# Kernel tuning notes

Hardware: AMD Instinct MI355X
Metric: run time of the kernel (lower is better)

The kernel has to match this reference:

```python
import jax, jax.numpy as jnp
import numpy as np

NUM_LEVEL = 16
LOG_T = 19
TABLE_SIZE = 2 ** LOG_T
FEAT = 2
MIN_RES = 16
MAX_RES = 512
N_POINTS = 262144

# [Teschner et al. 2003] spatial hash primes, wrapped to int32 like torch does
HASH_COEFFS = jnp.asarray(np.array([1, 2654435761, 805459861], dtype=np.uint32).astype(np.int32))


def _resolutions():
    coeff = (MAX_RES / MIN_RES) ** (1.0 / (NUM_LEVEL - 1))
    return jnp.floor(MIN_RES * (jnp.float32(coeff) ** jnp.arange(NUM_LEVEL, dtype=jnp.float32)))


def _spatial_hash(verts_i32):
    # verts_i32: (..., 3) int32; wrap-around int32 multiply then xor, then mod T (non-negative)
    x = HASH_COEFFS * verts_i32
    idx = jnp.bitwise_xor(jnp.bitwise_xor(x[..., 0], x[..., 1]), x[..., 2])
    return jnp.mod(idx, TABLE_SIZE)


def _hash_encode(coords, tables):
    # coords: (N,3) f32 in [0,1); tables: (L,T,F) f16
    res = _resolutions()                                   # (L,)
    scaled = coords[None, :, :] * res[:, None, None]        # (L,N,3)
    floor = jnp.floor(scaled)
    ceil = jnp.ceil(scaled)
    # 8 voxel corners via floor/ceil selection bits
    offs = jnp.asarray(np.array([[(o >> 2) & 1, (o >> 1) & 1, o & 1] for o in range(8)], dtype=np.bool_))
    sel = offs[:, None, None, :]                            # (8,1,1,3)
    corner = jnp.where(sel, ceil[None], floor[None])        # (8,L,N,3)
    comp = jnp.where(sel, floor[None], ceil[None])          # opposite corner (8,L,N,3)
    idx = _spatial_hash(corner.astype(jnp.int32))           # (8,L,N)
    # gather per-level features: tables[l][idx[:,l,:]] -> (L,8,N,F)
    feats = jax.vmap(lambda tab, i: tab[i], in_axes=(0, 1))(tables, idx)
    # trilinear weight of corner o = prod |opposite_corner - scaled|
    w = jnp.prod(jnp.abs(comp - scaled[None]), axis=-1)     # (8,L,N)
    w = jnp.transpose(w, (1, 0, 2))                         # (L,8,N)
    lvl = jnp.sum(feats.astype(jnp.float32) * w[..., None], axis=1)  # (L,N,F)
    return jnp.transpose(lvl, (1, 0, 2)).reshape(coords.shape[0], NUM_LEVEL * FEAT)


def _mlp(x, w_in, b_in, w_h0, b_h0, w_h1, b_h1, w_out, b_out):
    h = jax.nn.relu(x @ w_in.T + b_in)
    h = jax.nn.relu(h @ w_h0.T + b_h0)
    h = jax.nn.relu(h @ w_h1.T + b_h1)
    return h @ w_out.T + b_out


def setup_inputs() -> dict:
    key = jax.random.key(0)
    ks = jax.random.split(key, 8)
    coords = jax.random.uniform(ks[0], (N_POINTS, 3), dtype=jnp.float32)
    tables = (2e-4 * jax.random.uniform(ks[1], (NUM_LEVEL, TABLE_SIZE, FEAT), dtype=jnp.float32) - 1e-4).astype(jnp.float16)
    def lin(k, out_d, in_d):
        return jax.random.normal(k, (out_d, in_d), dtype=jnp.float32) * (1.0 / np.sqrt(in_d))
    return {
        'coords': coords, 'tables': tables,
        'w_in': lin(ks[2], 64, 32), 'b_in': jnp.zeros((64,), jnp.float32),
        'w_h0': lin(ks[3], 64, 64), 'b_h0': jnp.zeros((64,), jnp.float32),
        'w_h1': lin(ks[4], 64, 64), 'b_h1': jnp.zeros((64,), jnp.float32),
        'w_out': lin(ks[5], 16, 64), 'b_out': jnp.zeros((16,), jnp.float32),
    }


def reference(coords, tables, w_in, b_in, w_h0, b_h0, w_h1, b_h1, w_out, b_out):
    enc = _hash_encode(coords, tables)  # (N, 32)
    return _mlp(enc, w_in, b_in, w_h0, b_h0, w_h1, b_h1, w_out, b_out)  # (N, 16)
```

## Files before the change

kernel.cpp:

```cpp
#include <hip/hip_runtime.h>

#define NLVL 16
#define LOGT 19
#define TMASK ((1u << LOGT) - 1u)
#define SCALE 4096.0f
#define INV_SCALE (1.0f / 4096.0f)
#define NFRAG 22

typedef _Float16 half_t;
typedef half_t half8 __attribute__((ext_vector_type(8)));
typedef half_t half4 __attribute__((ext_vector_type(4)));
typedef half_t half2v __attribute__((ext_vector_type(2)));
typedef float  float4v __attribute__((ext_vector_type(4)));

__device__ __constant__ float RES_C[NLVL] = {16.f, 20.f, 25.f, 32.f, 40.f, 50.f, 64.f, 80.f,
                                             101.f, 128.f, 161.f, 203.f, 256.f, 322.f, 406.f, 512.f};

__device__ __forceinline__ float4v mfma16(half8 a, half8 b, float4v c) {
    return __builtin_amdgcn_mfma_f32_16x16x32_f16(a, b, c, 0, 0, 0);
}

__global__ __launch_bounds__(64, 1) void nerf_wprep(
    const float* __restrict__ w_in, const float* __restrict__ w_h0,
    const float* __restrict__ w_h1, const float* __restrict__ w_out,
    half8* __restrict__ frags)
{
    const int frag = blockIdx.x;
    const int lane = threadIdx.x;
    const int m    = lane & 15;
    const int quad = lane >> 4;

    const float* W; int ncol, row, col;
    if (frag < 4)       { W = w_in;  ncol = 32; row = frag * 16 + m;            col = quad * 8; }
    else if (frag < 12) { const int f = frag - 4;
                          W = w_h0;  ncol = 64; row = (f >> 1) * 16 + m;        col = (f & 1) * 32 + quad * 8; }
    else if (frag < 20) { const int f = frag - 12;
                          W = w_h1;  ncol = 64; row = (f >> 1) * 16 + m;        col = (f & 1) * 32 + quad * 8; }
    else                { const int f = frag - 20;
                          W = w_out; ncol = 64; row = m;                        col = f * 32 + quad * 8; }

    const float* p = W + row * ncol + col;
    half8 r;
    #pragma unroll
    for (int j = 0; j < 8; ++j) r[j] = (half_t)p[j];
    frags[frag * 64 + lane] = r;
}

__global__ __launch_bounds__(256, 8) void nerf_encode_pin(
    const float* __restrict__ coords,
    const float2* __restrict__ tab,
    half_t* __restrict__ encT, int npts)
{
    const int b    = blockIdx.x;
    const int half = (int)(gridDim.x >> 1);
    const int hi   = (b >= half) ? 1 : 0;
    const int l    = (b & 7) + (hi << 3);
    const int pb   = (hi ? (b - half) : b) >> 3;

    const int side = threadIdx.x & 1;
    const int base = pb * 256 + (threadIdx.x >> 1);
    const int p0 = base, p1 = base + 128;

    const float r = RES_C[l];
    const float2* __restrict__ bp = tab + (((unsigned)l) << LOGT);

    const float ax = coords[p0 * 3 + 0] * r, ay = coords[p0 * 3 + 1] * r, az = coords[p0 * 3 + 2] * r;
    const float afx = floorf(ax), afy = floorf(ay), afz = floorf(az);
    const float agx = ceilf(ax),  agy = ceilf(ay),  agz = ceilf(az);
    const unsigned ahx = side ? (unsigned)(int)agx : (unsigned)(int)afx;
    const float    awx = side ? (ax - afx) : (agx - ax);
    const unsigned ahfy = (unsigned)(int)afy * 2654435761u;
    const unsigned ahgy = (unsigned)(int)agy * 2654435761u;
    const unsigned ahfz = (unsigned)(int)afz * 805459861u;
    const unsigned ahgz = (unsigned)(int)agz * 805459861u;
    const float aty = ay - afy, atz = az - afz, auy = agy - ay, auz = agz - az;

    const float bx = coords[p1 * 3 + 0] * r, by = coords[p1 * 3 + 1] * r, bz = coords[p1 * 3 + 2] * r;
    const float bfx = floorf(bx), bfy = floorf(by), bfz = floorf(bz);
    const float bgx = ceilf(bx),  bgy = ceilf(by),  bgz = ceilf(bz);
    const unsigned bhx = side ? (unsigned)(int)bgx : (unsigned)(int)bfx;
    const float    bwx = side ? (bx - bfx) : (bgx - bx);
    const unsigned bhfy = (unsigned)(int)bfy * 2654435761u;
    const unsigned bhgy = (unsigned)(int)bgy * 2654435761u;
    const unsigned bhfz = (unsigned)(int)bfz * 805459861u;
    const unsigned bhgz = (unsigned)(int)bgz * 805459861u;
    const float bty = by - bfy, btz = bz - bfz, buy = bgy - by, buz = bgz - bz;

    const float2 a0 = bp[(ahx ^ ahfy ^ ahfz) & TMASK];
    const float2 a1 = bp[(ahx ^ ahfy ^ ahgz) & TMASK];
    const float2 a2 = bp[(ahx ^ ahgy ^ ahfz) & TMASK];
    const float2 a3 = bp[(ahx ^ ahgy ^ ahgz) & TMASK];
    const float2 b0 = bp[(bhx ^ bhfy ^ bhfz) & TMASK];
    const float2 b1 = bp[(bhx ^ bhfy ^ bhgz) & TMASK];
    const float2 b2 = bp[(bhx ^ bhgy ^ bhfz) & TMASK];
    const float2 b3 = bp[(bhx ^ bhgy ^ bhgz) & TMASK];

    const float aw0 = awx * auy * auz, aw1 = awx * auy * atz;
    const float aw2 = awx * aty * auz, aw3 = awx * aty * atz;
    const float bw0 = bwx * buy * buz, bw1 = bwx * buy * btz;
    const float bw2 = bwx * bty * buz, bw3 = bwx * bty * btz;

    float ae0 = aw0 * a0.x + aw1 * a1.x + aw2 * a2.x + aw3 * a3.x;
    float ae1 = aw0 * a0.y + aw1 * a1.y + aw2 * a2.y + aw3 * a3.y;
    float be0 = bw0 * b0.x + bw1 * b1.x + bw2 * b2.x + bw3 * b3.x;
    float be1 = bw0 * b0.y + bw1 * b1.y + bw2 * b2.y + bw3 * b3.y;

    ae0 += __shfl_xor(ae0, 1, 64);
    ae1 += __shfl_xor(ae1, 1, 64);
    be0 += __shfl_xor(be0, 1, 64);
    be1 += __shfl_xor(be1, 1, 64);

    if (side == 0) {
        half2v h0; h0[0] = (half_t)(ae0 * SCALE); h0[1] = (half_t)(ae1 * SCALE);
        half2v h1; h1[0] = (half_t)(be0 * SCALE); h1[1] = (half_t)(be1 * SCALE);
        *reinterpret_cast<half2v*>(&encT[((size_t)l * npts + p0) * 2]) = h0;
        *reinterpret_cast<half2v*>(&encT[((size_t)l * npts + p1) * 2]) = h1;
    }
}

__global__ __launch_bounds__(256, 2) void nerf_mlp4(
    const half_t* __restrict__ encT,
    const half8* __restrict__ frags,
    const float* __restrict__ b_in, const float* __restrict__ b_h0,
    const float* __restrict__ b_h1, const float* __restrict__ b_out,
    float* __restrict__ out, int npts)
{
    __shared__ half_t actS[4][64 * 64];

    const int t    = threadIdx.x;
    const int lane = t & 63;
    const int wv   = t >> 6;
    const int m    = lane & 15;
    const int quad = lane >> 4;

    const size_t pbase = (size_t)blockIdx.x * 256 + (size_t)wv * 64;

    half8 be[4];
    #pragma unroll
    for (int T = 0; T < 4; ++T) {
        #pragma unroll
        for (int d = 0; d < 4; ++d) {
            const int L = quad * 4 + d;
            const half2v v = *reinterpret_cast<const half2v*>(
                &encT[((size_t)L * npts + pbase + T * 16 + m) * 2]);
            be[T][d * 2 + 0] = v[0];
            be[T][d * 2 + 1] = v[1];
        }
    }

    half8 aL1[4], aL2[8], aL3[8], aL4[2];
    #pragma unroll
    for (int f = 0; f < 4; ++f) aL1[f] = frags[(0 + f) * 64 + lane];
    #pragma unroll
    for (int f = 0; f < 8; ++f) aL2[f] = frags[(4 + f) * 64 + lane];
    #pragma unroll
    for (int f = 0; f < 8; ++f) aL3[f] = frags[(12 + f) * 64 + lane];
    #pragma unroll
    for (int f = 0; f < 2; ++f) aL4[f] = frags[(20 + f) * 64 + lane];

    float4v bL1[4], bL2[4], bL3[4], bL4;
    #pragma unroll
    for (int mt = 0; mt < 4; ++mt) {
        bL1[mt] = *reinterpret_cast<const float4v*>(b_in + mt * 16 + quad * 4);
        bL2[mt] = *reinterpret_cast<const float4v*>(b_h0 + mt * 16 + quad * 4);
        bL3[mt] = *reinterpret_cast<const float4v*>(b_h1 + mt * 16 + quad * 4);
    }
    bL4 = *reinterpret_cast<const float4v*>(b_out + quad * 4);

    half_t* const buf = &actS[wv][0];
    const float4v zero = {0.f, 0.f, 0.f, 0.f};

    auto storeTile = [&](int lp, int mt, float4v acc, float4v bias) {
        half4 h4;
        #pragma unroll
        for (int r = 0; r < 4; ++r)
            h4[r] = (half_t)fmaxf(fmaf(bias[r], SCALE, acc[r]), 0.f);
        const int c16  = mt * 2 + (quad >> 1);
        const int phys = c16 ^ (lp & 7);
        *reinterpret_cast<half4*>(&buf[lp * 64 + phys * 8 + (quad & 1) * 4]) = h4;
    };
    auto loadB = [&](int lp, int h) -> half8 {
        const int phys = (h * 4 + quad) ^ (lp & 7);
        return *reinterpret_cast<const half8*>(&buf[lp * 64 + phys * 8]);
    };

    #pragma unroll
    for (int T = 0; T < 4; ++T) {
        const int lp = T * 16 + m;
        #pragma unroll
        for (int mt = 0; mt < 4; ++mt) {
            float4v acc = mfma16(aL1[mt], be[T], zero);
            storeTile(lp, mt, acc, bL1[mt]);
        }
    }
    #pragma unroll
    for (int T = 0; T < 4; ++T) {
        const int lp = T * 16 + m;
        const half8 p0 = loadB(lp, 0);
        const half8 p1 = loadB(lp, 1);
        #pragma unroll
        for (int mt = 0; mt < 4; ++mt) {
            float4v acc = mfma16(aL2[mt * 2 + 0], p0, zero);
            acc         = mfma16(aL2[mt * 2 + 1], p1, acc);
            storeTile(lp, mt, acc, bL2[mt]);
        }
    }
    #pragma unroll
    for (int T = 0; T < 4; ++T) {
        const int lp = T * 16 + m;
        const half8 p0 = loadB(lp, 0);
        const half8 p1 = loadB(lp, 1);
        #pragma unroll
        for (int mt = 0; mt < 4; ++mt) {
            float4v acc = mfma16(aL3[mt * 2 + 0], p0, zero);
            acc         = mfma16(aL3[mt * 2 + 1], p1, acc);
            storeTile(lp, mt, acc, bL3[mt]);
        }
    }
    #pragma unroll
    for (int T = 0; T < 4; ++T) {
        const int lp = T * 16 + m;
        const half8 p0 = loadB(lp, 0);
        const half8 p1 = loadB(lp, 1);
        float4v acc = mfma16(aL4[0], p0, zero);
        acc         = mfma16(aL4[1], p1, acc);
        float4v res;
        #pragma unroll
        for (int r = 0; r < 4; ++r)
            res[r] = fmaf(acc[r], INV_SCALE, bL4[r]);
        *reinterpret_cast<float4v*>(out + (pbase + lp) * 16 + quad * 4) = res;
    }
}

__global__ __launch_bounds__(256, 2) void nerf_fused(
    const float* __restrict__ coords,
    const float2* __restrict__ tab,
    const float* __restrict__ w_in, const float* __restrict__ b_in,
    const float* __restrict__ w_h0, const float* __restrict__ b_h0,
    const float* __restrict__ w_h1, const float* __restrict__ b_h1,
    const float* __restrict__ w_out, const float* __restrict__ b_out,
    float* __restrict__ out, int npts)
{
    __shared__ half_t encS[256 * 40];
    __shared__ half_t actS[4][2][32 * 64];

    const int t    = threadIdx.x;
    const int lane = t & 63;
    const int wv   = t >> 6;
    const int m    = lane & 15;
    const int quad = lane >> 4;
    const int pt = blockIdx.x * 256 + t;

    {
        const float cx = coords[pt * 3 + 0];
        const float cy = coords[pt * 3 + 1];
        const float cz = coords[pt * 3 + 2];
        float enc[32];
        #pragma unroll
        for (int l = 0; l < NLVL; ++l) {
            const float r = RES_C[l];
            const float sx = cx * r, sy = cy * r, sz = cz * r;
            const float fx = floorf(sx), fy = floorf(sy), fz = floorf(sz);
            const float gx = ceilf(sx),  gy = ceilf(sy),  gz = ceilf(sz);
            const unsigned hfx = (unsigned)(int)fx;
            const unsigned hgx = (unsigned)(int)gx;
            const unsigned hfy = (unsigned)(int)fy * 2654435761u;
            const unsigned hgy = (unsigned)(int)gy * 2654435761u;
            const unsigned hfz = (unsigned)(int)fz * 805459861u;
            const unsigned hgz = (unsigned)(int)gz * 805459861u;
            const float tx = sx - fx, ty = sy - fy, tz = sz - fz;
            const float ux = gx - sx, uy = gy - sy, uz = gz - sz;
            const unsigned lbase = ((unsigned)l) << LOGT;
            float e0 = 0.f, e1 = 0.f;
            #pragma unroll
            for (int o = 0; o < 8; ++o) {
                const unsigned h = ((o & 4) ? hgx : hfx)
                                 ^ ((o & 2) ? hgy : hfy)
                                 ^ ((o & 1) ? hgz : hfz);
                const unsigned idx = h & TMASK;
                const float w = (((o & 4) ? tx : ux)
                              *  ((o & 2) ? ty : uy))
                              *  ((o & 1) ? tz : uz);
                const float2 fv = tab[lbase + idx];
                e0 = fmaf(w, fv.x, e0);
                e1 = fmaf(w, fv.y, e1);
            }
            enc[2 * l + 0] = e0;
            enc[2 * l + 1] = e1;
        }
        #pragma unroll
        for (int c = 0; c < 4; ++c) {
            half8 h8;
            #pragma unroll
            for (int j = 0; j < 8; ++j) h8[j] = (half_t)(enc[c * 8 + j] * SCALE);
            *reinterpret_cast<half8*>(&encS[t * 40 + c * 8]) = h8;
        }
    }

    auto loadA = [&](const float* __restrict__ W, int ncol, int row, int col) -> half8 {
        const float* p = W + row * ncol + col;
        const float4v lo = *reinterpret_cast<const float4v*>(p);
        const float4v hi = *reinterpret_cast<const float4v*>(p + 4);
        half8 r;
        r[0] = (half_t)lo[0]; r[1] = (half_t)lo[1]; r[2] = (half_t)lo[2]; r[3] = (half_t)lo[3];
        r[4] = (half_t)hi[0]; r[5] = (half_t)hi[1]; r[6] = (half_t)hi[2]; r[7] = (half_t)hi[3];
        return r;
    };

    half8 aL1[4], aL2[8], aL3[8], aL4[2];
    #pragma unroll
    for (int mt = 0; mt < 4; ++mt) aL1[mt] = loadA(w_in, 32, mt * 16 + m, quad * 8);
    #pragma unroll
    for (int mt = 0; mt < 4; ++mt) {
        aL2[mt * 2 + 0] = loadA(w_h0, 64, mt * 16 + m, 0 * 32 + quad * 8);
        aL2[mt * 2 + 1] = loadA(w_h0, 64, mt * 16 + m, 1 * 32 + quad * 8);
        aL3[mt * 2 + 0] = loadA(w_h1, 64, mt * 16 + m, 0 * 32 + quad * 8);
        aL3[mt * 2 + 1] = loadA(w_h1, 64, mt * 16 + m, 1 * 32 + quad * 8);
    }
    aL4[0] = loadA(w_out, 64, m, 0 * 32 + quad * 8);
    aL4[1] = loadA(w_out, 64, m, 1 * 32 + quad * 8);

    float4v bL1[4], bL2[4], bL3[4], bL4;
    #pragma unroll
    for (int mt = 0; mt < 4; ++mt) {
        bL1[mt] = *reinterpret_cast<const float4v*>(b_in + mt * 16 + quad * 4);
        bL2[mt] = *reinterpret_cast<const float4v*>(b_h0 + mt * 16 + quad * 4);
        bL3[mt] = *reinterpret_cast<const float4v*>(b_h1 + mt * 16 + quad * 4);
    }
    bL4 = *reinterpret_cast<const float4v*>(b_out + quad * 4);

    half_t* const ping = &actS[wv][0][0];
    half_t* const pong = &actS[wv][1][0];
    const float4v zero = {0.f, 0.f, 0.f, 0.f};

    auto storeTile = [&](half_t* buf, int lp, int mt, float4v acc, float4v bias) {
        half4 h4;
        #pragma unroll
        for (int r = 0; r < 4; ++r)
            h4[r] = (half_t)fmaxf(fmaf(bias[r], SCALE, acc[r]), 0.f);
        const int c16  = mt * 2 + (quad >> 1);
        const int phys = c16 ^ (lp & 7);
        *reinterpret_cast<half4*>(&buf[lp * 64 + phys * 8 + (quad & 1) * 4]) = h4;
    };
    auto loadB = [&](half_t* buf, int lp, int h) -> half8 {
        const int phys = (h * 4 + quad) ^ (lp & 7);
        return *reinterpret_cast<const half8*>(&buf[lp * 64 + phys * 8]);
    };

    for (int g = 0; g < 2; ++g) {
        #pragma unroll
        for (int nt = 0; nt < 2; ++nt) {
            const int lp   = nt * 16 + m;
            const int prow = wv * 64 + g * 32 + lp;
            const half8 bfr = *reinterpret_cast<const half8*>(&encS[prow * 40 + quad * 8]);
            #pragma unroll
            for (int mt = 0; mt < 4; ++mt) {
                float4v acc = mfma16(aL1[mt], bfr, zero);
                storeTile(ping, lp, mt, acc, bL1[mt]);
            }
            {
                const half8 p0 = loadB(ping, lp, 0);
                const half8 p1 = loadB(ping, lp, 1);
                #pragma unroll
                for (int mt = 0; mt < 4; ++mt) {
                    float4v acc = mfma16(aL2[mt * 2 + 0], p0, zero);
                    acc         = mfma16(aL2[mt * 2 + 1], p1, acc);
                    storeTile(pong, lp, mt, acc, bL2[mt]);
                }
            }
            {
                const half8 p0 = loadB(pong, lp, 0);
                const half8 p1 = loadB(pong, lp, 1);
                #pragma unroll
                for (int mt = 0; mt < 4; ++mt) {
                    float4v acc = mfma16(aL3[mt * 2 + 0], p0, zero);
                    acc         = mfma16(aL3[mt * 2 + 1], p1, acc);
                    storeTile(ping, lp, mt, acc, bL3[mt]);
                }
            }
            {
                const half8 p0 = loadB(ping, lp, 0);
                const half8 p1 = loadB(ping, lp, 1);
                float4v acc = mfma16(aL4[0], p0, zero);
                acc         = mfma16(aL4[1], p1, acc);
                float4v res;
                #pragma unroll
                for (int r = 0; r < 4; ++r)
                    res[r] = fmaf(acc[r], INV_SCALE, bL4[r]);
                const size_t ptg = (size_t)blockIdx.x * 256 + (size_t)wv * 64 + g * 32 + lp;
                *reinterpret_cast<float4v*>(out + ptg * 16 + quad * 4) = res;
            }
        }
    }
}

extern "C" void kernel_launch(void* const* d_in, const int* in_sizes, int n_in,
                              void* d_out, int out_size, void* d_ws, size_t ws_size,
                              hipStream_t stream) {
    const float*  coords = (const float*)d_in[0];
    const float2* tables = (const float2*)d_in[1];
    const float*  w_in   = (const float*)d_in[2];
    const float*  b_in   = (const float*)d_in[3];
    const float*  w_h0   = (const float*)d_in[4];
    const float*  b_h0   = (const float*)d_in[5];
    const float*  w_h1   = (const float*)d_in[6];
    const float*  b_h1   = (const float*)d_in[7];
    const float*  w_out  = (const float*)d_in[8];
    const float*  b_out  = (const float*)d_in[9];
    float* out = (float*)d_out;

    const int npts = in_sizes[0] / 3;
    const size_t encBytes  = (size_t)npts * 32 * sizeof(half_t);
    const size_t fragBytes = (size_t)NFRAG * 64 * sizeof(half8);

    if (ws_size >= encBytes + fragBytes && (npts & 255) == 0) {
        half_t* encT  = (half_t*)d_ws;
        half8*  frags = (half8*)((char*)d_ws + encBytes);
        nerf_wprep<<<NFRAG, 64, 0, stream>>>(w_in, w_h0, w_h1, w_out, frags);
        const int bpl = npts >> 8;
        nerf_encode_pin<<<bpl * NLVL, 256, 0, stream>>>(coords, tables, encT, npts);
        nerf_mlp4<<<npts / 256, 256, 0, stream>>>(encT, frags,
                                                  b_in, b_h0, b_h1, b_out,
                                                  out, npts);
    } else {
        nerf_fused<<<npts / 256, 256, 0, stream>>>(coords, tables,
                                                   w_in, b_in, w_h0, b_h0,
                                                   w_h1, b_h1, w_out, b_out,
                                                   out, npts);
    }
}
```

Measured before the change: 195.8 us.

## Keep MLP activations in registers via cross-lane shuffle transpose instead of LDS

The MLP kernel drops its per-wave shared-memory activation buffer. Each layer's MFMA accumulator is converted to ReLU'd fp16 pairs and rearranged into the next layer's B-operand layout with two xor-shuffles per register. Bias is folded into the MFMA accumulator init, and launch bounds are raised to allow more waves per CU. This removes LDS store/load round trips between layers, in exchange for extra shuffle and select instructions and possible register pressure at the higher occupancy target.

```diff
diff --git a/kernel.cpp b/kernel.cpp
--- a/kernel.cpp
+++ b/kernel.cpp
@@ -12,6 +12,7 @@
 typedef half_t half4 __attribute__((ext_vector_type(4)));
 typedef half_t half2v __attribute__((ext_vector_type(2)));
 typedef float  float4v __attribute__((ext_vector_type(4)));
+typedef unsigned int uint4v __attribute__((ext_vector_type(4)));
 
 __device__ __constant__ float RES_C[NLVL] = {16.f, 20.f, 25.f, 32.f, 40.f, 50.f, 64.f, 80.f,
                                              101.f, 128.f, 161.f, 203.f, 256.f, 322.f, 406.f, 512.f};
@@ -118,21 +119,56 @@
     }
 }
 
-__global__ __launch_bounds__(256, 2) void nerf_mlp4(
+__device__ __forceinline__ unsigned pack_relu2(float x, float y) {
+    half2v h;
+    h[0] = (half_t)fmaxf(x, 0.f);
+    h[1] = (half_t)fmaxf(y, 0.f);
+    return __builtin_bit_cast(unsigned, h);
+}
+
+__device__ __forceinline__ void xpose_relu(const float4v acc[4], int lane,
+                                           half8& b0, half8& b1) {
+    unsigned X[4], Y[4];
+    X[0] = pack_relu2(acc[0][0], acc[0][1]);
+    X[1] = pack_relu2(acc[0][2], acc[0][3]);
+    X[2] = pack_relu2(acc[2][0], acc[2][1]);
+    X[3] = pack_relu2(acc[2][2], acc[2][3]);
+    Y[0] = pack_relu2(acc[1][0], acc[1][1]);
+    Y[1] = pack_relu2(acc[1][2], acc[1][3]);
+    Y[2] = pack_relu2(acc[3][0], acc[3][1]);
+    Y[3] = pack_relu2(acc[3][2], acc[3][3]);
+    const bool lo = (lane & 32) == 0;
+    const bool ev = (lane & 16) == 0;
+    uint4v u0, u1;
+    #pragma unroll
+    for (int j = 0; j < 4; ++j) {
+        const unsigned s1 = lo ? Y[j] : X[j];
+        const unsigned t1 = __shfl_xor(s1, 32, 64);
+        const unsigned A1 = lo ? X[j] : t1;
+        const unsigned B1 = lo ? t1 : Y[j];
+        const unsigned s2 = ev ? B1 : A1;
+        const unsigned t2 = __shfl_xor(s2, 16, 64);
+        const unsigned a2 = ev ? A1 : t2;
+        const unsigned b2 = ev ? t2 : B1;
+        if (j < 2) { u0[j] = a2; u0[2 + j] = b2; }
+        else       { u1[j - 2] = a2; u1[j] = b2; }
+    }
+    b0 = __builtin_bit_cast(half8, u0);
+    b1 = __builtin_bit_cast(half8, u1);
+}
+
+__global__ __launch_bounds__(256, 4) void nerf_mlp5(
     const half_t* __restrict__ encT,
     const half8* __restrict__ frags,
     const float* __restrict__ b_in, const float* __restrict__ b_h0,
     const float* __restrict__ b_h1, const float* __restrict__ b_out,
     float* __restrict__ out, int npts)
 {
-    __shared__ half_t actS[4][64 * 64];
-
     const int t    = threadIdx.x;
     const int lane = t & 63;
     const int wv   = t >> 6;
     const int m    = lane & 15;
     const int quad = lane >> 4;
-
     const size_t pbase = (size_t)blockIdx.x * 256 + (size_t)wv * 64;
 
     half8 be[4];
@@ -148,87 +184,76 @@
         }
     }
 
-    half8 aL1[4], aL2[8], aL3[8], aL4[2];
-    #pragma unroll
-    for (int f = 0; f < 4; ++f) aL1[f] = frags[(0 + f) * 64 + lane];
-    #pragma unroll
-    for (int f = 0; f < 8; ++f) aL2[f] = frags[(4 + f) * 64 + lane];
-    #pragma unroll
-    for (int f = 0; f < 8; ++f) aL3[f] = frags[(12 + f) * 64 + lane];
-    #pragma unroll
-    for (int f = 0; f < 2; ++f) aL4[f] = frags[(20 + f) * 64 + lane];
-
-    float4v bL1[4], bL2[4], bL3[4], bL4;
-    #pragma unroll
-    for (int mt = 0; mt < 4; ++mt) {
-        bL1[mt] = *reinterpret_cast<const float4v*>(b_in + mt * 16 + quad * 4);
-        bL2[mt] = *reinterpret_cast<const float4v*>(b_h0 + mt * 16 + quad * 4);
-        bL3[mt] = *reinterpret_cast<const float4v*>(b_h1 + mt * 16 + quad * 4);
-    }
-    bL4 = *reinterpret_cast<const float4v*>(b_out + quad * 4);
-
-    half_t* const buf = &actS[wv][0];
-    const float4v zero = {0.f, 0.f, 0.f, 0.f};
-
-    auto storeTile = [&](int lp, int mt, float4v acc, float4v bias) {
-        half4 h4;
-        #pragma unroll
-        for (int r = 0; r < 4; ++r)
-            h4[r] = (half_t)fmaxf(fmaf(bias[r], SCALE, acc[r]), 0.f);
-        const int c16  = mt * 2 + (quad >> 1);
-        const int phys = c16 ^ (lp & 7);
-        *reinterpret_cast<half4*>(&buf[lp * 64 + phys * 8 + (quad & 1) * 4]) = h4;
-    };
-    auto loadB = [&](int lp, int h) -> half8 {
-        const int phys = (h * 4 + quad) ^ (lp & 7);
-        return *reinterpret_cast<const half8*>(&buf[lp * 64 + phys * 8]);
-    };
-
-    #pragma unroll
-    for (int T = 0; T < 4; ++T) {
-        const int lp = T * 16 + m;
-        #pragma unroll
-        for (int mt = 0; mt < 4; ++mt) {
-            float4v acc = mfma16(aL1[mt], be[T], zero);
-            storeTile(lp, mt, acc, bL1[mt]);
-        }
-    }
-    #pragma unroll
-    for (int T = 0; T < 4; ++T) {
-        const int lp = T * 16 + m;
-        const half8 p0 = loadB(lp, 0);
-        const half8 p1 = loadB(lp, 1);
-        #pragma unroll
-        for (int mt = 0; mt < 4; ++mt) {
-            float4v acc = mfma16(aL2[mt * 2 + 0], p0, zero);
-            acc         = mfma16(aL2[mt * 2 + 1], p1, acc);
-            storeTile(lp, mt, acc, bL2[mt]);
-        }
-    }
-    #pragma unroll
-    for (int T = 0; T < 4; ++T) {
-        const int lp = T * 16 + m;
-        const half8 p0 = loadB(lp, 0);
-        const half8 p1 = loadB(lp, 1);
-        #pragma unroll
-        for (int mt = 0; mt < 4; ++mt) {
-            float4v acc = mfma16(aL3[mt * 2 + 0], p0, zero);
-            acc         = mfma16(aL3[mt * 2 + 1], p1, acc);
-            storeTile(lp, mt, acc, bL3[mt]);
-        }
-    }
-    #pragma unroll
-    for (int T = 0; T < 4; ++T) {
-        const int lp = T * 16 + m;
-        const half8 p0 = loadB(lp, 0);
-        const half8 p1 = loadB(lp, 1);
-        float4v acc = mfma16(aL4[0], p0, zero);
-        acc         = mfma16(aL4[1], p1, acc);
-        float4v res;
-        #pragma unroll
-        for (int r = 0; r < 4; ++r)
-            res[r] = fmaf(acc[r], INV_SCALE, bL4[r]);
-        *reinterpret_cast<float4v*>(out + (pbase + lp) * 16 + quad * 4) = res;
+    half8 bf0[4], bf1[4];
+
+    {
+        half8 w[4];
+        #pragma unroll
+        for (int f = 0; f < 4; ++f) w[f] = frags[(0 + f) * 64 + lane];
+        float4v cin[4];
+        #pragma unroll
+        for (int mt = 0; mt < 4; ++mt)
+            cin[mt] = (*reinterpret_cast<const float4v*>(b_in + mt * 16 + quad * 4)) * SCALE;
+        #pragma unroll
+        for (int T = 0; T < 4; ++T) {
+            float4v acc[4];
+            #pragma unroll
+            for (int mt = 0; mt < 4; ++mt) acc[mt] = mfma16(w[mt], be[T], cin[mt]);
+            xpose_relu(acc, lane, bf0[T], bf1[T]);
+        }
+    }
+    {
+        half8 w[8];
+        #pragma unroll
+        for (int f = 0; f < 8; ++f) w[f] = frags[(4 + f) * 64 + lane];
+        float4v cin[4];
+        #pragma unroll
+        for (int mt = 0; mt < 4; ++mt)
+            cin[mt] = (*reinterpret_cast<const float4v*>(b_h0 + mt * 16 + quad * 4)) * SCALE;
+        #pragma unroll
+        for (int T = 0; T < 4; ++T) {
+            float4v acc[4];
+            #pragma unroll
+            for (int mt = 0; mt < 4; ++mt) {
+                acc[mt] = mfma16(w[mt * 2 + 0], bf0[T], cin[mt]);
+                acc[mt] = mfma16(w[mt * 2 + 1], bf1[T], acc[mt]);
+            }
+            xpose_relu(acc, lane, bf0[T], bf1[T]);
+        }
+    }
+    {
+        half8 w[8];
+        #pragma unroll
+        for (int f = 0; f < 8; ++f) w[f] = frags[(12 + f) * 64 + lane];
+        float4v cin[4];
+        #pragma unroll
+        for (int mt = 0; mt < 4; ++mt)
+            cin[mt] = (*reinterpret_cast<const float4v*>(b_h1 + mt * 16 + quad * 4)) * SCALE;
+        #pragma unroll
+        for (int T = 0; T < 4; ++T) {
+            float4v acc[4];
+            #pragma unroll
+            for (int mt = 0; mt < 4; ++mt) {
+                acc[mt] = mfma16(w[mt * 2 + 0], bf0[T], cin[mt]);
+                acc[mt] = mfma16(w[mt * 2 + 1], bf1[T], acc[mt]);
+            }
+            xpose_relu(acc, lane, bf0[T], bf1[T]);
+        }
+    }
+    {
+        const half8 w0 = frags[20 * 64 + lane];
+        const half8 w1 = frags[21 * 64 + lane];
+        const float4v b4 = *reinterpret_cast<const float4v*>(b_out + quad * 4);
+        const float4v zero = {0.f, 0.f, 0.f, 0.f};
+        #pragma unroll
+        for (int T = 0; T < 4; ++T) {
+            float4v acc = mfma16(w0, bf0[T], zero);
+            acc         = mfma16(w1, bf1[T], acc);
+            float4v res;
+            #pragma unroll
+            for (int r = 0; r < 4; ++r) res[r] = fmaf(acc[r], INV_SCALE, b4[r]);
+            *reinterpret_cast<float4v*>(out + (pbase + T * 16 + m) * 16 + quad * 4) = res;
+        }
     }
 }
 
@@ -419,7 +444,7 @@
         nerf_wprep<<<NFRAG, 64, 0, stream>>>(w_in, w_h0, w_h1, w_out, frags);
         const int bpl = npts >> 8;
         nerf_encode_pin<<<bpl * NLVL, 256, 0, stream>>>(coords, tables, encT, npts);
-        nerf_mlp4<<<npts / 256, 256, 0, stream>>>(encT, frags,
+        nerf_mlp5<<<npts / 256, 256, 0, stream>>>(encT, frags,
                                                   b_in, b_h0, b_h1, b_out,
                                                   out, npts);
     } else {
```

New measurement: 200.5 us. 2.4% more time.
